# Kernel optimization log

Measured on AMD Instinct MI355X. Metric: run time of the kernel, lower is better.

The kernel has to match this reference:

```python
import jax, jax.numpy as jnp
import numpy as np

B, T, H = 128, 1024, 200
IN0, OUT = 8, 4  # GRU layer-0 input size (4 targets + 4 emotion), fc output dim


def setup_inputs() -> dict:
    key = jax.random.key(0)
    ks = jax.random.split(key, 12)
    s = 1.0 / np.sqrt(H)  # torch RNN default init: U(-1/sqrt(H), 1/sqrt(H))
    u = lambda k, shp: jax.random.uniform(k, shp, jnp.float32, -s, s)
    return {
        "x": jax.random.normal(ks[0], (B, T, IN0), jnp.float32),
        "W_ih0": u(ks[1], (3 * H, IN0)),
        "W_hh0": u(ks[2], (3 * H, H)),
        "b_ih0": u(ks[3], (3 * H,)),
        "b_hh0": u(ks[4], (3 * H,)),
        "W_ih1": u(ks[5], (3 * H, H)),
        "W_hh1": u(ks[6], (3 * H, H)),
        "b_ih1": u(ks[7], (3 * H,)),
        "b_hh1": u(ks[8], (3 * H,)),
        "W_fc": u(ks[9], (OUT, H)),
        "b_fc": u(ks[10], (OUT,)),
        "xlens": jax.random.randint(ks[11], (B,), 1, T + 1),
    }


def _gru_cell(h, gx, W_hh, b_hh):
    # torch GRU cell: gx = W_ih @ x + b_ih precomputed, gates order [r, z, n]
    gh = h @ W_hh.T + b_hh
    ir, iz, i_n = jnp.split(gx, 3, axis=-1)
    hr, hz, hn = jnp.split(gh, 3, axis=-1)
    r = jax.nn.sigmoid(ir + hr)
    z = jax.nn.sigmoid(iz + hz)
    n = jnp.tanh(i_n + r * hn)
    return (1.0 - z) * n + z * h


def _forward(x, W_ih0, W_hh0, b_ih0, b_hh0, W_ih1, W_hh1, b_ih1, b_hh1, W_fc, b_fc):
    b, t, _ = x.shape
    emotion = x[:, 0, -4:]                      # (B,4) frozen at t=0, as in source
    targets = x[:, :, :4]                       # (B,T,4)
    # step inputs: t=0 -> ones(B,4); t>0 -> targets[:, t-1] (teacher forcing)
    tf = jnp.concatenate([jnp.ones((b, 1, 4), x.dtype), targets[:, :-1, :]], axis=1)
    inputs = jnp.concatenate(
        [tf, jnp.broadcast_to(emotion[:, None, :], (b, t, 4))], axis=-1)  # (B,T,8)
    # precompute layer-0 input projections for all steps (one big GEMM)
    gx0 = jnp.einsum("btc,gc->btg", inputs, W_ih0) + b_ih0  # (B,T,3H)

    def step(carry, gx0_t):
        h0, h1 = carry
        h0 = _gru_cell(h0, gx0_t, W_hh0, b_hh0)
        gx1 = h0 @ W_ih1.T + b_ih1
        h1 = _gru_cell(h1, gx1, W_hh1, b_hh1)
        out = jnp.tanh(h1 @ W_fc.T + b_fc)      # fused fc + tanh
        return (h0, h1), out

    h0 = jnp.zeros((b, H), x.dtype)
    h1 = jnp.zeros((b, H), x.dtype)
    _, outs = jax.lax.scan(step, (h0, h1), jnp.swapaxes(gx0, 0, 1))  # (T,B,4)
    return jnp.swapaxes(outs, 0, 1)             # (B,T,4)


def reference(x, W_ih0, W_hh0, b_ih0, b_hh0, W_ih1, W_hh1, b_ih1, b_hh1, W_fc, b_fc, xlens):
    # xlens is accepted but unused, exactly as in the source forward()
    return _forward(x, W_ih0, W_hh0, b_ih0, b_hh0, W_ih1, W_hh1, b_ih1, b_hh1, W_fc, b_fc)
```

## Files before the change

### kernel.cpp

```cpp
#include <hip/hip_runtime.h>
#include <hip/hip_bf16.h>


#define TT 1024
#define HH 200
#define NB 16
#define HS 13
#define KP 232

typedef __attribute__((ext_vector_type(8))) short short8;
typedef __attribute__((ext_vector_type(4))) float f32x4;

__device__ __forceinline__ float sigm(float v) { return 1.0f / (1.0f + __expf(-v)); }
__device__ __forceinline__ float tanh_fast(float v) {
  float e = __expf(-2.0f * v);
  return (1.0f - e) / (1.0f + e);
}
__device__ __forceinline__ uint llc_load_u32(const uint* p) {
  return __hip_atomic_load(p, __ATOMIC_RELAXED, __HIP_MEMORY_SCOPE_SYSTEM);
}
__device__ __forceinline__ void llc_store_u32(uint* p, uint v) {
  __hip_atomic_store(p, v, __ATOMIC_RELAXED, __HIP_MEMORY_SCOPE_SYSTEM);
}
__device__ __forceinline__ float bfu2f(ushort u) {
  return __uint_as_float(((uint)u) << 16);
}
__device__ __forceinline__ ushort f2bfu(float f) {
  __hip_bfloat16 b = __float2bfloat16(f);
  return *(ushort*)&b;
}
__device__ __forceinline__ uint packf(float h) {
  ushort hi = f2bfu(h);
  float  fh = bfu2f(hi);
  ushort lo = f2bfu(h - fh);
  return (uint)hi | ((uint)lo << 16);
}

__global__ __launch_bounds__(256, 1) void gru2_mfma(
    const float* __restrict__ x,
    const float* __restrict__ Wih0, const float* __restrict__ Whh0,
    const float* __restrict__ bih0, const float* __restrict__ bhh0,
    const float* __restrict__ Wih1, const float* __restrict__ Whh1,
    const float* __restrict__ bih1, const float* __restrict__ bhh1,
    const float* __restrict__ Wfc,  const float* __restrict__ bfc,
    float* __restrict__ out,
    uint* __restrict__ h0g, uint* __restrict__ h1g, int* __restrict__ bars)
{
  __shared__ __align__(16) ushort hBh[2][NB][KP];
  __shared__ __align__(16) ushort hBl[2][NB][KP];
  __shared__ float D[117][17];
  __shared__ float Wi0[39][8];
  __shared__ float bi0[39], bh0[39], bi1[39], bh1[39], bfs[4];
  __shared__ float xc[NB][8];

  const int tid  = threadIdx.x;
  const int wave = tid >> 6;
  const int lane = tid & 63;
  const int m15  = lane & 15;
  const int q    = lane >> 4;

  const int g  = blockIdx.x & 7;
  const int s  = blockIdx.x >> 3;
  const int b0 = g * NB;
  const int j0 = s * HS;
  const int hs = (HH - j0 < HS) ? (HH - j0) : HS;
  const int th   = 3 * hs;
  const int h0r  = 6 * hs;
  const int T0   = (h0r + 15) >> 4;
  const int NT   = T0 + ((th + 15) >> 4);
  const bool isOut = (s == 15);

  short8 Ah[2][7], Al[2][7];
  #pragma unroll
  for (int mt = 0; mt < 2; ++mt) {
    const int T = wave * 2 + mt;
    const bool fc  = isOut && (wave == 2) && (mt == 0);
    const bool val = fc || (T < NT);
    #pragma unroll
    for (int kt = 0; kt < 7; ++kt) {
      short8 vh = {0,0,0,0,0,0,0,0}, vl = {0,0,0,0,0,0,0,0};
      #pragma unroll
      for (int j = 0; j < 8; ++j) {
        const int k = kt * 32 + q * 8 + j;
        float w = 0.0f;
        if (val && k < HH) {
          if (fc) {
            if (m15 < 4) w = Wfc[m15 * HH + k];
          } else {
            const int p = T * 16 + m15;
            int r = -1;
            if (p < h0r) r = p;
            else if (p >= T0 * 16 && (p - T0 * 16) < th) r = h0r + (p - T0 * 16);
            if (r >= 0) {
              const int m  = r / th, rr = r - m * th;
              const int qq = rr / hs, jj = rr - qq * hs;
              const float* src = (m == 0) ? Whh0 : ((m == 1) ? Wih1 : Whh1);
              w = src[(qq * HH + j0 + jj) * HH + k];
            }
          }
        }
        const ushort uh = f2bfu(w);
        const ushort ul = f2bfu(w - bfu2f(uh));
        vh[j] = (short)uh; vl[j] = (short)ul;
      }
      Ah[mt][kt] = vh; Al[mt][kt] = vl;
    }
  }

  for (int u = tid; u < th * 8; u += 256) {
    int rr = u >> 3, c = u & 7;
    int qq = rr / hs, jj = rr - qq * hs;
    Wi0[rr][c] = Wih0[(qq * HH + j0 + jj) * 8 + c];
  }
  for (int u = tid; u < th; u += 256) {
    int qq = u / hs, jj = u - qq * hs;
    int grow = qq * HH + j0 + jj;
    bi0[u] = bih0[grow]; bh0[u] = bhh0[grow];
    bi1[u] = bih1[grow]; bh1[u] = bhh1[grow];
  }
  if (tid < 4) bfs[tid] = bfc[tid];
  for (int u = tid; u < 2 * NB * KP / 2; u += 256) ((uint*)hBh)[u] = 0;
  for (int u = tid; u < 2 * NB * KP / 2; u += 256) ((uint*)hBl)[u] = 0;
  __syncthreads();

  int* bar = &bars[g * 64];
  const int cj = tid >> 4, cb = tid & 15;

  for (int t = 0; t <= TT + 1; ++t) {
    const uint* h0src = h0g + ((t + 1) & 1) * (128 * HH);
    const uint* h1src = h1g + (t & 1) * (128 * HH);
    uint tmp[25];
    #pragma unroll
    for (int i = 0; i < 25; ++i) {
      const int u  = tid + i * 256;
      const int st = u / 3200, rem = u - st * 3200;
      const int b  = rem / 200, k = rem - b * 200;
      tmp[i] = llc_load_u32(&(st ? h1src : h0src)[(b0 + b) * HH + k]);
    }
    #pragma unroll
    for (int i = 0; i < 25; ++i) {
      const int u  = tid + i * 256;
      const int st = u / 3200, rem = u - st * 3200;
      const int b  = rem / 200, k = rem - b * 200;
      hBh[st][b][k] = (ushort)(tmp[i] & 0xffff);
      hBl[st][b][k] = (ushort)(tmp[i] >> 16);
    }
    if (tid < 128 && t < TT) {
      int b = tid >> 3, c = tid & 7;
      float v;
      if (c < 4) v = (t == 0) ? 1.0f : x[((b0 + b) * TT + (t - 1)) * 8 + c];
      else       v = x[(b0 + b) * TT * 8 + c];
      xc[b][c] = v;
    }
    __syncthreads();

    #pragma unroll
    for (int mt = 0; mt < 2; ++mt) {
      const int T = wave * 2 + mt;
      const bool fc  = isOut && (wave == 2) && (mt == 0);
      const bool val = fc || (T < NT);
      if (!val) continue;
      const int st = fc ? 1 : ((T < T0) ? 0 : 1);
      const ushort* Bh = &hBh[st][m15][0];
      const ushort* Bl = &hBl[st][m15][0];
      f32x4 acc = {0.f, 0.f, 0.f, 0.f};
      #pragma unroll
      for (int kt = 0; kt < 7; ++kt) {
        const short8 bh = *(const short8*)&Bh[kt * 32 + q * 8];
        const short8 bl = *(const short8*)&Bl[kt * 32 + q * 8];
        acc = __builtin_amdgcn_mfma_f32_16x16x32_bf16(Ah[mt][kt], bh, acc, 0, 0, 0);
        acc = __builtin_amdgcn_mfma_f32_16x16x32_bf16(Ah[mt][kt], bl, acc, 0, 0, 0);
        acc = __builtin_amdgcn_mfma_f32_16x16x32_bf16(Al[mt][kt], bh, acc, 0, 0, 0);
      }
      if (fc) {
        if (t >= 2) {
          #pragma unroll
          for (int i = 0; i < 4; ++i) {
            const int p = q * 4 + i;
            if (p < 4)
              out[((b0 + m15) * TT + (t - 2)) * 4 + p] = tanh_fast(acc[i] + bfs[p]);
          }
        }
      } else {
        #pragma unroll
        for (int i = 0; i < 4; ++i) {
          const int p = T * 16 + q * 4 + i;
          int r = -1;
          if (p < h0r) r = p;
          else if (p >= T0 * 16 && (p - T0 * 16) < th) r = h0r + (p - T0 * 16);
          if (r >= 0) D[r][m15] = acc[i];
        }
      }
    }
    __syncthreads();

    if (cj < hs) {
      const float hv0 = bfu2f(hBh[0][cb][j0 + cj]) + bfu2f(hBl[0][cb][j0 + cj]);
      const float hv1 = bfu2f(hBh[1][cb][j0 + cj]) + bfu2f(hBl[1][cb][j0 + cj]);
      if (t < TT) {
        float ir = bi0[cj], iz = bi0[hs + cj], in_ = bi0[2 * hs + cj];
        #pragma unroll
        for (int c = 0; c < 8; ++c) {
          const float xv = xc[cb][c];
          ir  += Wi0[cj][c] * xv;
          iz  += Wi0[hs + cj][c] * xv;
          in_ += Wi0[2 * hs + cj][c] * xv;
        }
        const float hr = D[cj][cb] + bh0[cj];
        const float hz = D[hs + cj][cb] + bh0[hs + cj];
        const float hn = D[2 * hs + cj][cb] + bh0[2 * hs + cj];
        const float r = sigm(ir + hr), z = sigm(iz + hz);
        const float n = tanh_fast(in_ + r * hn);
        llc_store_u32(&h0g[(t & 1) * (128 * HH) + (b0 + cb) * HH + j0 + cj],
                      packf((1.0f - z) * n + z * hv0));
      }
      if (t >= 1 && t <= TT) {
        const float ir  = D[3 * hs + cj][cb] + bi1[cj];
        const float iz  = D[4 * hs + cj][cb] + bi1[hs + cj];
        const float in_ = D[5 * hs + cj][cb] + bi1[2 * hs + cj];
        const float hr  = D[6 * hs + cj][cb] + bh1[cj];
        const float hz  = D[7 * hs + cj][cb] + bh1[hs + cj];
        const float hn  = D[8 * hs + cj][cb] + bh1[2 * hs + cj];
        const float r = sigm(ir + hr), z = sigm(iz + hz);
        const float n = tanh_fast(in_ + r * hn);
        llc_store_u32(&h1g[((t + 1) & 1) * (128 * HH) + (b0 + cb) * HH + j0 + cj],
                      packf((1.0f - z) * n + z * hv1));
      }
    }

    __syncthreads();
    if (tid == 0) {
      __hip_atomic_fetch_add(bar, 1, __ATOMIC_RELAXED, __HIP_MEMORY_SCOPE_SYSTEM);
      const int target = 16 * (t + 1);
      while (__hip_atomic_load(bar, __ATOMIC_RELAXED, __HIP_MEMORY_SCOPE_SYSTEM) < target)
        __builtin_amdgcn_s_sleep(1);
    }
    __syncthreads();
  }
}

extern "C" void kernel_launch(void* const* d_in, const int* in_sizes, int n_in,
                              void* d_out, int out_size, void* d_ws, size_t ws_size,
                              hipStream_t stream) {
  uint* ws = (uint*)d_ws;
  hipMemsetAsync(d_ws, 0, (size_t)(102400 + 512) * sizeof(uint), stream);
  gru2_mfma<<<128, 256, 0, stream>>>(
      (const float*)d_in[0],
      (const float*)d_in[1], (const float*)d_in[2],
      (const float*)d_in[3], (const float*)d_in[4],
      (const float*)d_in[5], (const float*)d_in[6],
      (const float*)d_in[7], (const float*)d_in[8],
      (const float*)d_in[9], (const float*)d_in[10],
      (float*)d_out, ws, ws + 51200, (int*)(ws + 102400));
}
```

Before: 3.157 ms.

## Replace block-level atomic barrier with per-wave flag barrier and prefetch inputs

Each wave now publishes its step counter into a per-wave flag slot, then polls all 64 flags of its group with one lane per flag and exits once every flag has caught up. This replaces the syncthreads plus single-thread atomic counter barrier. The point is to drop two block-wide syncthreads and the serialized atomic add per timestep. The emotion part of x is loaded once up front and the teacher-forcing value is loaded early in each step to hide its latency. The risks are the bounded spin count, which can break out early and break correctness, and the loss of the block-wide sync that used to order shared memory reuse between steps.

```diff
diff --git a/kernel.cpp b/kernel.cpp
--- a/kernel.cpp
+++ b/kernel.cpp
@@ -44,7 +44,7 @@
     const float* __restrict__ bih1, const float* __restrict__ bhh1,
     const float* __restrict__ Wfc,  const float* __restrict__ bfc,
     float* __restrict__ out,
-    uint* __restrict__ h0g, uint* __restrict__ h1g, int* __restrict__ bars)
+    uint* __restrict__ h0g, uint* __restrict__ h1g, uint* __restrict__ syncp)
 {
   __shared__ __align__(16) ushort hBh[2][NB][KP];
   __shared__ __align__(16) ushort hBl[2][NB][KP];
@@ -69,6 +69,8 @@
   const int T0   = (h0r + 15) >> 4;
   const int NT   = T0 + ((th + 15) >> 4);
   const bool isOut = (s == 15);
+
+  uint* flags = syncp;
 
   short8 Ah[2][7], Al[2][7];
   #pragma unroll
@@ -121,12 +123,18 @@
   if (tid < 4) bfs[tid] = bfc[tid];
   for (int u = tid; u < 2 * NB * KP / 2; u += 256) ((uint*)hBh)[u] = 0;
   for (int u = tid; u < 2 * NB * KP / 2; u += 256) ((uint*)hBl)[u] = 0;
+  if (tid < 128 && (tid & 7) >= 4)
+    xc[tid >> 3][tid & 7] = x[(b0 + (tid >> 3)) * TT * 8 + (tid & 7)];
   __syncthreads();
 
-  int* bar = &bars[g * 64];
   const int cj = tid >> 4, cb = tid & 15;
+  const int xb = tid >> 3, xcc7 = tid & 7;
 
   for (int t = 0; t <= TT + 1; ++t) {
+    float xtf = 1.0f;
+    if (tid < 128 && xcc7 < 4 && t > 0 && t < TT)
+      xtf = x[((b0 + xb) * TT + (t - 1)) * 8 + xcc7];
+
     const uint* h0src = h0g + ((t + 1) & 1) * (128 * HH);
     const uint* h1src = h1g + (t & 1) * (128 * HH);
     uint tmp[25];
@@ -145,13 +153,8 @@
       hBh[st][b][k] = (ushort)(tmp[i] & 0xffff);
       hBl[st][b][k] = (ushort)(tmp[i] >> 16);
     }
-    if (tid < 128 && t < TT) {
-      int b = tid >> 3, c = tid & 7;
-      float v;
-      if (c < 4) v = (t == 0) ? 1.0f : x[((b0 + b) * TT + (t - 1)) * 8 + c];
-      else       v = x[(b0 + b) * TT * 8 + c];
-      xc[b][c] = v;
-    }
+    if (tid < 128 && xcc7 < 4 && t < TT)
+      xc[xb][xcc7] = xtf;
     __syncthreads();
 
     #pragma unroll
@@ -228,14 +231,20 @@
       }
     }
 
-    __syncthreads();
-    if (tid == 0) {
-      __hip_atomic_fetch_add(bar, 1, __ATOMIC_RELAXED, __HIP_MEMORY_SCOPE_SYSTEM);
-      const int target = 16 * (t + 1);
-      while (__hip_atomic_load(bar, __ATOMIC_RELAXED, __HIP_MEMORY_SCOPE_SYSTEM) < target)
+    {
+      const uint tgt = (uint)(t + 1);
+      asm volatile("s_waitcnt vmcnt(0)" ::: "memory");
+      if (lane == 0)
+        llc_store_u32(&flags[g * 64 + s * 4 + wave], tgt);
+      const int own = s * 4 + wave;
+      const uint* fp = &flags[g * 64 + lane];
+      for (int it = 0; it < 30000; ++it) {
+        uint v = tgt;
+        if (lane != own) v = llc_load_u32(fp);
+        if (__all((int)(v >= tgt))) break;
         __builtin_amdgcn_s_sleep(1);
-    }
-    __syncthreads();
+      }
+    }
   }
 }
 
@@ -251,5 +260,5 @@
       (const float*)d_in[5], (const float*)d_in[6],
       (const float*)d_in[7], (const float*)d_in[8],
       (const float*)d_in[9], (const float*)d_in[10],
-      (float*)d_out, ws, ws + 51200, (int*)(ws + 102400));
-}
+      (float*)d_out, ws, ws + 51200, ws + 102400);
+}
```

New measurement: 8.058 ms. 2.55x slower.
